# Kernel tuning notes

Measured on AMD Instinct MI355X. Metric: run time of the kernel, lower is better.

## Reference

```python
import jax, jax.numpy as jnp
import numpy as np

C = 256
K = 8
CQK = C // K  # 32 query/key channels


def setup_inputs() -> dict:
    key = jax.random.key(0)
    ks = jax.random.split(key, 10)
    B, H, W = 8, 64, 64
    s = 0.02
    return {
        "x": jax.random.normal(ks[0], (B, C, H, W), jnp.float32),
        "Wf": jax.random.normal(ks[1], (CQK, C), jnp.float32) * s,
        "bf": jax.random.normal(ks[2], (CQK,), jnp.float32) * s,
        "Wg": jax.random.normal(ks[3], (CQK, C), jnp.float32) * s,
        "bg": jax.random.normal(ks[4], (CQK,), jnp.float32) * s,
        "Wh": jax.random.normal(ks[5], (C, C), jnp.float32) * s,
        "bh": jax.random.normal(ks[6], (C,), jnp.float32) * s,
        "Wv": jax.random.normal(ks[7], (C, C), jnp.float32) * s,
        "bv": jax.random.normal(ks[8], (C,), jnp.float32) * s,
        "gamma": jax.random.normal(ks[9], (1,), jnp.float32) * 0.1,
    }


def _conv1x1(x, W, b):
    # x: [B,C,H,W], W: [O,C] -> [B,O,H,W]
    return jnp.einsum("oc,bchw->bohw", W, x) + b[None, :, None, None]


def reference(x, Wf, bf, Wg, bg, Wh, bh, Wv, bv, gamma):
    B, Cc, Hd, Wd = x.shape
    N = Hd * Wd
    f = _conv1x1(x, Wf, bf).reshape(B, CQK, N)   # keys of query i
    g = _conv1x1(x, Wg, bg).reshape(B, CQK, N)
    h = _conv1x1(x, Wh, bh).reshape(B, Cc, N)
    # att[b,i,j] = softmax_j( f_i . g_j )
    att = jnp.einsum("bci,bcj->bij", f, g)       # [B,N,N]
    att = jax.nn.softmax(att, axis=-1)
    # out[b,c,i] = sum_j h[b,c,j] * att[b,i,j]
    att_h = jnp.einsum("bcj,bij->bci", h, att).reshape(B, Cc, Hd, Wd)
    att_h = _conv1x1(att_h, Wv, bv)
    return x + gamma[0] * att_h
```

## Files before the change

kernel.cpp:

```cpp
#include <hip/hip_runtime.h>
#include <hip/hip_bf16.h>
#include <stdint.h>

#define BATCH 8
#define CH    256
#define CQK   32
#define NPIX  4096
#define MALL  320

using bfrag = __attribute__((ext_vector_type(8))) short;
using f32x4 = __attribute__((ext_vector_type(4))) float;
using u32x2 = __attribute__((ext_vector_type(2))) unsigned int;

#define MFMA16(A, B, C) __builtin_amdgcn_mfma_f32_16x16x32_bf16(A, B, C, 0, 0, 0)

#if __has_builtin(__builtin_amdgcn_exp2f)
#define EXP2(x) __builtin_amdgcn_exp2f(x)
#else
#define EXP2(x) exp2f(x)
#endif

__device__ __forceinline__ unsigned short f2bf(float f) {
  union { float f; unsigned int u; } v; v.f = f;
  unsigned int r = v.u + 0x7FFFu + ((v.u >> 16) & 1u);
  return (unsigned short)(r >> 16);
}

__device__ __forceinline__ void gload_lds16(const void* g, void* l) {
  __builtin_amdgcn_global_load_lds(
      (const __attribute__((address_space(1))) unsigned int*)g,
      (__attribute__((address_space(3))) unsigned int*)l, 16, 0, 0);
}

__global__ void prep_kernel(const float* __restrict__ Wf, const float* __restrict__ Wg,
                            const float* __restrict__ Wh, const float* __restrict__ Wv,
                            unsigned short* __restrict__ Wall, unsigned short* __restrict__ Wvb) {
  int i = blockIdx.x * 256 + threadIdx.x;
  if (i < MALL * CH) {
    int m = i >> 8, c = i & 255;
    float v = (m < CQK)     ? Wf[m * CH + c]
            : (m < 2 * CQK) ? Wg[(m - CQK) * CH + c]
                            : Wh[(m - 2 * CQK) * CH + c];
    Wall[i] = f2bf(v);
  }
  if (i < CH * CH) Wvb[i] = f2bf(Wv[i]);
}

__global__ __launch_bounds__(256, 2)
void proj_kernel(const float* __restrict__ x, const unsigned short* __restrict__ Wall,
                 const float* __restrict__ bfb, const float* __restrict__ bgb,
                 const float* __restrict__ bhb,
                 unsigned short* __restrict__ Qo, unsigned short* __restrict__ Ko,
                 unsigned short* __restrict__ Vo) {
  __shared__ char xT[64 * 512];
  const int b  = blockIdx.x & 7;
  const int n0 = (blockIdx.x >> 3) * 64;
  const int tid = threadIdx.x;
  const int lane = tid & 63, wave = tid >> 6;
  const int lr = lane & 15, g = lane >> 4;

  for (int it = 0; it < 16; ++it) {
    int c = it * 16 + wave * 4 + g;
    int nn = lr * 4;
    const float4 v = *(const float4*)(x + (size_t)(b * CH + c) * NPIX + n0 + nn);
    const float* vp = (const float*)&v;
#pragma unroll
    for (int j = 0; j < 4; ++j) {
      int n = nn + j;
      int byteoff = n * 512 + (((c >> 3) ^ (n & 7)) << 4) + ((c & 7) * 2);
      *(unsigned short*)(xT + byteoff) = f2bf(vp[j]);
    }
  }
  __syncthreads();

  f32x4 acc[5][4] = {};
  for (int ks = 0; ks < 8; ++ks) {
    bfrag bfr[4];
#pragma unroll
    for (int nt = 0; nt < 4; ++nt) {
      int n = nt * 16 + lr;
      bfr[nt] = *(const bfrag*)(xT + n * 512 + (((ks * 4 + g) ^ (n & 7)) << 4));
    }
#pragma unroll
    for (int i = 0; i < 5; ++i) {
      int m = (wave + 4 * i) * 16 + lr;
      bfrag afr = *(const bfrag*)(Wall + (size_t)m * CH + ks * 32 + g * 8);
#pragma unroll
      for (int nt = 0; nt < 4; ++nt) acc[i][nt] = MFMA16(afr, bfr[nt], acc[i][nt]);
    }
  }

  const float L2E = 1.4426950408889634f;
#pragma unroll
  for (int i = 0; i < 5; ++i) {
    const int mt = wave + 4 * i;
#pragma unroll
    for (int nt = 0; nt < 4; ++nt) {
      const int n = n0 + nt * 16 + lr;
      if (mt < 2) {
        float v0 = (acc[i][nt][0] + bfb[mt * 16 + 4 * g + 0]) * L2E;
        float v1 = (acc[i][nt][1] + bfb[mt * 16 + 4 * g + 1]) * L2E;
        float v2 = (acc[i][nt][2] + bfb[mt * 16 + 4 * g + 2]) * L2E;
        float v3 = (acc[i][nt][3] + bfb[mt * 16 + 4 * g + 3]) * L2E;
        u32x2 pk;
        pk[0] = (unsigned)f2bf(v0) | ((unsigned)f2bf(v1) << 16);
        pk[1] = (unsigned)f2bf(v2) | ((unsigned)f2bf(v3) << 16);
        *(u32x2*)(Qo + (size_t)(b * NPIX + n) * CQK + mt * 16 + 4 * g) = pk;
      } else if (mt < 4) {
        int k0 = (mt - 2) * 16 + 4 * g;
        float v0 = acc[i][nt][0] + bgb[k0 + 0];
        float v1 = acc[i][nt][1] + bgb[k0 + 1];
        float v2 = acc[i][nt][2] + bgb[k0 + 2];
        float v3 = acc[i][nt][3] + bgb[k0 + 3];
        u32x2 pk;
        pk[0] = (unsigned)f2bf(v0) | ((unsigned)f2bf(v1) << 16);
        pk[1] = (unsigned)f2bf(v2) | ((unsigned)f2bf(v3) << 16);
        *(u32x2*)(Ko + (size_t)(b * NPIX + n) * CQK + k0) = pk;
      } else {
#pragma unroll
        for (int r = 0; r < 4; ++r) {
          int c = mt * 16 + 4 * g + r - 64;
          Vo[(size_t)(b * CH + c) * NPIX + n] = f2bf(acc[i][nt][r] + bhb[c]);
        }
      }
    }
  }
}

__global__ __launch_bounds__(256)
void attn_kernel(const unsigned short* __restrict__ Qg, const unsigned short* __restrict__ Kg,
                 const unsigned short* __restrict__ Vg, unsigned short* __restrict__ Og) {
  __shared__ char Pb[8192];

  const int b  = blockIdx.x & 7;
  const int q0 = (blockIdx.x >> 3) * 64;
  const int tid = threadIdx.x;
  const int lane = tid & 63, wave = tid >> 6;
  const int lr = lane & 15, g = lane >> 4;

  const unsigned short* Qbase = Qg + (size_t)(b * NPIX + q0) * CQK;
  const unsigned short* Kfp   = Kg + (size_t)b * NPIX * CQK + (size_t)(16 * wave + lr) * CQK + g * 8;
  const unsigned short* Vfp   = Vg + (size_t)b * CH * NPIX + g * 8;

  bfrag qf[4];
#pragma unroll
  for (int nt = 0; nt < 4; ++nt)
    qf[nt] = *(const bfrag*)(Qbase + (nt * 16 + lr) * CQK + g * 8);

  f32x4 acc[4][4] = {};
  float lp[4] = {0.f, 0.f, 0.f, 0.f};
  const int pwG = 2 * wave + (g >> 1);

  bfrag kf = *(const bfrag*)(Kfp);

  for (int t = 0; t < 64; ++t) {
    bfrag vf[2][4];
#pragma unroll
    for (int ks = 0; ks < 2; ++ks)
#pragma unroll
      for (int nt = 0; nt < 4; ++nt)
        vf[ks][nt] = *(const bfrag*)(Vfp + (size_t)(64 * wave + nt * 16 + lr) * NPIX
                                         + t * 64 + ks * 32);

#pragma unroll
    for (int nt = 0; nt < 4; ++nt) {
      f32x4 zero = {0.f, 0.f, 0.f, 0.f};
      f32x4 st = MFMA16(kf, qf[nt], zero);
      float p0 = EXP2(st[0]), p1 = EXP2(st[1]);
      float p2 = EXP2(st[2]), p3 = EXP2(st[3]);
      lp[nt] += (p0 + p1) + (p2 + p3);
      union { float f; unsigned u; } u0, u1, u2, u3;
      u0.f = p0; u1.f = p1; u2.f = p2; u3.f = p3;
      u32x2 pk;
      pk[0] = ((u0.u + 0x8000u) >> 16) | ((u1.u + 0x8000u) & 0xFFFF0000u);
      pk[1] = ((u2.u + 0x8000u) >> 16) | ((u3.u + 0x8000u) & 0xFFFF0000u);
      int q = nt * 16 + lr;
      *(u32x2*)(Pb + q * 128 + ((pwG ^ (q & 7)) << 4) + ((g & 1) << 3)) = pk;
    }

    kf = *(const bfrag*)(Kfp + (size_t)(((t + 1) & 63) * 64) * CQK);

    asm volatile("s_waitcnt lgkmcnt(0)" ::: "memory");
    __builtin_amdgcn_s_barrier();

#pragma unroll
    for (int ks = 0; ks < 2; ++ks) {
      bfrag pf[4];
#pragma unroll
      for (int mt = 0; mt < 4; ++mt) {
        int q = mt * 16 + lr;
        pf[mt] = *(const bfrag*)(Pb + q * 128 + (((ks * 4 + g) ^ (q & 7)) << 4));
      }
#pragma unroll
      for (int mt = 0; mt < 4; ++mt)
#pragma unroll
        for (int nt = 0; nt < 4; ++nt)
          acc[mt][nt] = MFMA16(pf[mt], vf[ks][nt], acc[mt][nt]);
    }

    asm volatile("s_waitcnt lgkmcnt(0)" ::: "memory");
    __builtin_amdgcn_s_barrier();
  }

#pragma unroll
  for (int nt = 0; nt < 4; ++nt) {
    lp[nt] += __shfl_xor(lp[nt], 16);
    lp[nt] += __shfl_xor(lp[nt], 32);
  }
  float* lred = (float*)Pb;
  if (lane < 16) {
#pragma unroll
    for (int nt = 0; nt < 4; ++nt) lred[wave * 64 + nt * 16 + lr] = lp[nt];
  }
  __syncthreads();
  float inv[4][4];
#pragma unroll
  for (int mt = 0; mt < 4; ++mt)
#pragma unroll
    for (int r = 0; r < 4; ++r) {
      int q = mt * 16 + 4 * g + r;
      float s = lred[q] + lred[64 + q] + lred[128 + q] + lred[192 + q];
      inv[mt][r] = 1.0f / s;
    }
#pragma unroll
  for (int mt = 0; mt < 4; ++mt)
#pragma unroll
    for (int nt = 0; nt < 4; ++nt) {
      int c = 64 * wave + nt * 16 + lr;
#pragma unroll
      for (int r = 0; r < 4; ++r) {
        int q = q0 + mt * 16 + 4 * g + r;
        Og[(size_t)(b * NPIX + q) * CH + c] = f2bf(acc[mt][nt][r] * inv[mt][r]);
      }
    }
}

__global__ __launch_bounds__(256, 2)
void vproj_kernel(const unsigned short* __restrict__ attn, const unsigned short* __restrict__ Wvb,
                  const float* __restrict__ bv, const float* __restrict__ x,
                  const float* __restrict__ gamma, float* __restrict__ out) {
  __shared__ char at[64 * 512];
  const int b  = blockIdx.x & 7;
  const int n0 = (blockIdx.x >> 3) * 64;
  const int tid = threadIdx.x;
  const int lane = tid & 63, wave = tid >> 6;
  const int lr = lane & 15, g = lane >> 4;

#pragma unroll
  for (int i = 0; i < 8; ++i) {
    int ch = i * 256 + tid;
    int n = ch >> 5, G = ch & 31;
    gload_lds16(attn + (size_t)(b * NPIX + n0 + n) * CH + (G ^ (n & 7)) * 8,
                at + (i * 256 + wave * 64) * 16);
  }
  __syncthreads();

  f32x4 acc[4][4] = {};
  for (int ks = 0; ks < 8; ++ks) {
    bfrag bfr[4];
#pragma unroll
    for (int nt = 0; nt < 4; ++nt) {
      int n = nt * 16 + lr;
      bfr[nt] = *(const bfrag*)(at + n * 512 + (((ks * 4 + g) ^ (n & 7)) << 4));
    }
#pragma unroll
    for (int i = 0; i < 4; ++i) {
      int m = (wave * 4 + i) * 16 + lr;
      bfrag afr = *(const bfrag*)(Wvb + (size_t)m * CH + ks * 32 + g * 8);
#pragma unroll
      for (int nt = 0; nt < 4; ++nt) acc[i][nt] = MFMA16(afr, bfr[nt], acc[i][nt]);
    }
  }
  const float gam = gamma[0];
#pragma unroll
  for (int i = 0; i < 4; ++i)
#pragma unroll
    for (int nt = 0; nt < 4; ++nt) {
      int n = n0 + nt * 16 + lr;
#pragma unroll
      for (int r = 0; r < 4; ++r) {
        int m = (wave * 4 + i) * 16 + 4 * g + r;
        size_t off = (size_t)(b * CH + m) * NPIX + n;
        out[off] = x[off] + gam * (acc[i][nt][r] + bv[m]);
      }
    }
}

extern "C" void kernel_launch(void* const* d_in, const int* in_sizes, int n_in,
                              void* d_out, int out_size, void* d_ws, size_t ws_size,
                              hipStream_t stream) {
  const float* x   = (const float*)d_in[0];
  const float* Wf  = (const float*)d_in[1];
  const float* bfb = (const float*)d_in[2];
  const float* Wg  = (const float*)d_in[3];
  const float* bgb = (const float*)d_in[4];
  const float* Wh  = (const float*)d_in[5];
  const float* bhb = (const float*)d_in[6];
  const float* Wv  = (const float*)d_in[7];
  const float* bv  = (const float*)d_in[8];
  const float* gam = (const float*)d_in[9];
  float* out = (float*)d_out;

  char* ws = (char*)d_ws;
  unsigned short* Wall = (unsigned short*)(ws);
  unsigned short* Wvb  = (unsigned short*)(ws + 163840);
  unsigned short* Q    = (unsigned short*)(ws + 294912);
  unsigned short* K    = (unsigned short*)(ws + 2392064);
  unsigned short* V    = (unsigned short*)(ws + 4489216);
  unsigned short* attn = (unsigned short*)(ws + 21266432);

  prep_kernel<<<320, 256, 0, stream>>>(Wf, Wg, Wh, Wv, Wall, Wvb);
  proj_kernel<<<512, 256, 0, stream>>>(x, Wall, bfb, bgb, bhb, Q, K, V);
  attn_kernel<<<512, 256, 0, stream>>>(Q, K, V, attn);
  vproj_kernel<<<512, 256, 0, stream>>>(attn, Wvb, bv, x, gam, out);
}
```

Measured before the change: 176.0 us.

## Tile V into contiguous 64-pixel blocks and streamline attention inner loop

The projection kernel now writes V in a tiled layout in which each 64-pixel key tile of every channel is stored contiguously, so the attention kernel's per-iteration V fragment loads hit compact 128-byte rows instead of rows strided by the full pixel count. The attention loop also issues the next K fragment load earlier, precomputes the swizzled LDS offsets, uses the hardware packed bf16 conversion instruction, and adds sched_barriers around the workgroup barriers. The aim is better global-memory locality and fewer ALU instructions in the hot loop. Two things change numerically or in scheduling: the packed conversion rounds differently from the old manual rounding, and the sched_barriers restrict how the compiler can interleave instructions.

New measurement: 177.6 us. About the same (+0.9%).

```diff
diff --git a/kernel.cpp b/kernel.cpp
--- a/kernel.cpp
+++ b/kernel.cpp
@@ -51,7 +51,7 @@
                  const float* __restrict__ bfb, const float* __restrict__ bgb,
                  const float* __restrict__ bhb,
                  unsigned short* __restrict__ Qo, unsigned short* __restrict__ Ko,
-                 unsigned short* __restrict__ Vo) {
+                 unsigned short* __restrict__ Vp) {
   __shared__ char xT[64 * 512];
   const int b  = blockIdx.x & 7;
   const int n0 = (blockIdx.x >> 3) * 64;
@@ -91,12 +91,14 @@
   }
 
   const float L2E = 1.4426950408889634f;
+  const int vtile = (b * 64 + (n0 >> 6)) * 256;
 #pragma unroll
   for (int i = 0; i < 5; ++i) {
     const int mt = wave + 4 * i;
 #pragma unroll
     for (int nt = 0; nt < 4; ++nt) {
-      const int n = n0 + nt * 16 + lr;
+      const int nl = nt * 16 + lr;
+      const int n  = n0 + nl;
       if (mt < 2) {
         float v0 = (acc[i][nt][0] + bfb[mt * 16 + 4 * g + 0]) * L2E;
         float v1 = (acc[i][nt][1] + bfb[mt * 16 + 4 * g + 1]) * L2E;
@@ -120,7 +122,7 @@
 #pragma unroll
         for (int r = 0; r < 4; ++r) {
           int c = mt * 16 + 4 * g + r - 64;
-          Vo[(size_t)(b * CH + c) * NPIX + n] = f2bf(acc[i][nt][r] + bhb[c]);
+          Vp[(size_t)(vtile + c) * 64 + nl] = f2bf(acc[i][nt][r] + bhb[c]);
         }
       }
     }
@@ -129,7 +131,7 @@
 
 __global__ __launch_bounds__(256)
 void attn_kernel(const unsigned short* __restrict__ Qg, const unsigned short* __restrict__ Kg,
-                 const unsigned short* __restrict__ Vg, unsigned short* __restrict__ Og) {
+                 const unsigned short* __restrict__ Vp, unsigned short* __restrict__ Og) {
   __shared__ char Pb[8192];
 
   const int b  = blockIdx.x & 7;
@@ -139,8 +141,8 @@
   const int lr = lane & 15, g = lane >> 4;
 
   const unsigned short* Qbase = Qg + (size_t)(b * NPIX + q0) * CQK;
-  const unsigned short* Kfp   = Kg + (size_t)b * NPIX * CQK + (size_t)(16 * wave + lr) * CQK + g * 8;
-  const unsigned short* Vfp   = Vg + (size_t)b * CH * NPIX + g * 8;
+  const unsigned short* Kf    = Kg + (size_t)b * NPIX * CQK + (16 * wave + lr) * CQK + g * 8;
+  const unsigned short* Vf    = Vp + ((size_t)b * 64 * CH + 64 * wave + lr) * 64 + g * 8;
 
   bfrag qf[4];
 #pragma unroll
@@ -149,18 +151,22 @@
 
   f32x4 acc[4][4] = {};
   float lp[4] = {0.f, 0.f, 0.f, 0.f};
-  const int pwG = 2 * wave + (g >> 1);
-
-  bfrag kf = *(const bfrag*)(Kfp);
+  const int pwG   = 2 * wave + (g >> 1);
+  const int pwBase = lr * 128 + ((pwG ^ (lr & 7)) << 4) + ((g & 1) << 3);
+  const int prBase0 = lr * 128 + (((0 * 4 + g) ^ (lr & 7)) << 4);
+  const int prBase1 = lr * 128 + (((1 * 4 + g) ^ (lr & 7)) << 4);
+
+  bfrag kf = *(const bfrag*)(Kf);
 
   for (int t = 0; t < 64; ++t) {
     bfrag vf[2][4];
+    const unsigned short* vt = Vf + (size_t)t * CH * 64;
 #pragma unroll
     for (int ks = 0; ks < 2; ++ks)
 #pragma unroll
       for (int nt = 0; nt < 4; ++nt)
-        vf[ks][nt] = *(const bfrag*)(Vfp + (size_t)(64 * wave + nt * 16 + lr) * NPIX
-                                         + t * 64 + ks * 32);
+        vf[ks][nt] = *(const bfrag*)(vt + (nt * 16) * 64 + ks * 32);
+    bfrag kn = *(const bfrag*)(Kf + (size_t)(((t + 1) & 63) * 64) * CQK);
 
 #pragma unroll
     for (int nt = 0; nt < 4; ++nt) {
@@ -169,28 +175,25 @@
       float p0 = EXP2(st[0]), p1 = EXP2(st[1]);
       float p2 = EXP2(st[2]), p3 = EXP2(st[3]);
       lp[nt] += (p0 + p1) + (p2 + p3);
-      union { float f; unsigned u; } u0, u1, u2, u3;
-      u0.f = p0; u1.f = p1; u2.f = p2; u3.f = p3;
-      u32x2 pk;
-      pk[0] = ((u0.u + 0x8000u) >> 16) | ((u1.u + 0x8000u) & 0xFFFF0000u);
-      pk[1] = ((u2.u + 0x8000u) >> 16) | ((u3.u + 0x8000u) & 0xFFFF0000u);
-      int q = nt * 16 + lr;
-      *(u32x2*)(Pb + q * 128 + ((pwG ^ (q & 7)) << 4) + ((g & 1) << 3)) = pk;
-    }
-
-    kf = *(const bfrag*)(Kfp + (size_t)(((t + 1) & 63) * 64) * CQK);
+      unsigned lo, hi;
+      asm("v_cvt_pk_bf16_f32 %0, %1, %2" : "=v"(lo) : "v"(p0), "v"(p1));
+      asm("v_cvt_pk_bf16_f32 %0, %1, %2" : "=v"(hi) : "v"(p2), "v"(p3));
+      u32x2 pk; pk[0] = lo; pk[1] = hi;
+      *(u32x2*)(Pb + nt * 2048 + pwBase) = pk;
+    }
+    kf = kn;
 
     asm volatile("s_waitcnt lgkmcnt(0)" ::: "memory");
     __builtin_amdgcn_s_barrier();
+    __builtin_amdgcn_sched_barrier(0);
 
 #pragma unroll
     for (int ks = 0; ks < 2; ++ks) {
       bfrag pf[4];
-#pragma unroll
-      for (int mt = 0; mt < 4; ++mt) {
-        int q = mt * 16 + lr;
-        pf[mt] = *(const bfrag*)(Pb + q * 128 + (((ks * 4 + g) ^ (q & 7)) << 4));
-      }
+      const int prB = ks ? prBase1 : prBase0;
+#pragma unroll
+      for (int mt = 0; mt < 4; ++mt)
+        pf[mt] = *(const bfrag*)(Pb + mt * 2048 + prB);
 #pragma unroll
       for (int mt = 0; mt < 4; ++mt)
 #pragma unroll
@@ -200,6 +203,7 @@
 
     asm volatile("s_waitcnt lgkmcnt(0)" ::: "memory");
     __builtin_amdgcn_s_barrier();
+    __builtin_amdgcn_sched_barrier(0);
   }
 
 #pragma unroll
```
